# Kernel optimization log

Hardware: AMD Instinct MI355X
Metric: run time of the kernel (lower is better)

Reference implementation:

```python
import jax, jax.numpy as jnp
import numpy as np

B, T, D, H, F = 8, 1024, 512, 8, 2048
DK = D // H
EPS = 1e-3  # Keras LayerNormalization default epsilon
NEG = -1e9


def layer_norm(x, g, b):
    mu = jnp.mean(x, axis=-1, keepdims=True)
    var = jnp.mean(jnp.square(x - mu), axis=-1, keepdims=True)
    return (x - mu) * jax.lax.rsqrt(var + EPS) * g + b


def setup_inputs() -> dict:
    key = jax.random.key(0)
    ks = jax.random.split(key, 16)
    s = 1.0 / np.sqrt(D)
    sf = 1.0 / np.sqrt(F)
    x = jax.random.normal(ks[0], (B, T, D), dtype=jnp.float32)
    # binary attention mask (1 = attend). Random block-sparse-ish pattern.
    mask = (jax.random.uniform(ks[1], (B, 1, T, T)) > 0.15).astype(jnp.float32)
    return {
        "x": x,
        "mask": mask,
        "ln_in_g": jnp.ones((D,), jnp.float32),
        "ln_in_b": jnp.zeros((D,), jnp.float32),
        "Wq": jax.random.normal(ks[2], (D, D), jnp.float32) * s,
        "bq": jnp.zeros((D,), jnp.float32),
        "Wk": jax.random.normal(ks[3], (D, D), jnp.float32) * s,
        "bk": jnp.zeros((D,), jnp.float32),
        "Wv": jax.random.normal(ks[4], (D, D), jnp.float32) * s,
        "bv": jnp.zeros((D,), jnp.float32),
        "ln1_g": jnp.ones((D,), jnp.float32),
        "ln1_b": jnp.zeros((D,), jnp.float32),
        "W1": jax.random.normal(ks[5], (D, F), jnp.float32) * s,
        "b1": jnp.zeros((F,), jnp.float32),
        "W2": jax.random.normal(ks[6], (F, D), jnp.float32) * sf,
        "b2": jnp.zeros((D,), jnp.float32),
        "ln2_g": jnp.ones((D,), jnp.float32),
        "ln2_b": jnp.zeros((D,), jnp.float32),
    }


def reference(x, mask, ln_in_g, ln_in_b, Wq, bq, Wk, bk, Wv, bv,
              ln1_g, ln1_b, W1, b1, W2, b2, ln2_g, ln2_b):
    bs = x.shape[0]
    h = layer_norm(x, ln_in_g, ln_in_b)                      # [B,T,D]
    # QKV projections, split heads -> [B,H,T,DK]
    q = (h @ Wq + bq).reshape(bs, -1, H, DK).transpose(0, 2, 1, 3)
    k = (h @ Wk + bk).reshape(bs, -1, H, DK).transpose(0, 2, 1, 3)
    v = (h @ Wv + bv).reshape(bs, -1, H, DK).transpose(0, 2, 1, 3)
    scores = jnp.einsum('bhtd,bhsd->bhts', q, k) / np.sqrt(DK)
    scores = scores + NEG * (1.0 - mask)                     # additive mask
    probs = jax.nn.softmax(scores, axis=-1)                  # dropout: identity at inference
    attn = jnp.einsum('bhts,bhsd->bhtd', probs, v)
    attn = attn.transpose(0, 2, 1, 3).reshape(bs, -1, H * DK)
    # residual with ORIGINAL inputs (pre-ln_in), as in call() -> attend(inputs,...)
    attn = attn + x
    a = layer_norm(attn, ln1_g, ln1_b)
    f = jax.nn.relu(a @ W1 + b1) @ W2 + b2
    out = layer_norm(f + a, ln2_g, ln2_b)
    return out
```

## Files before the change

### kernel.cpp

```cpp
#include <hip/hip_runtime.h>

typedef unsigned short u16;
typedef unsigned long long u64;
typedef __bf16 bf16x8 __attribute__((ext_vector_type(8)));
typedef float f32x4 __attribute__((ext_vector_type(4)));

#define B_ 8
#define T_ 1024
#define D_ 512
#define H_ 8
#define DK_ 64
#define F_ 2048

__device__ __forceinline__ u16 f2bf(float f) {
    unsigned u = __float_as_uint(f);
    u += 0x7fffu + ((u >> 16) & 1u);
    return (u16)(u >> 16);
}

__global__ __launch_bounds__(256) void prep_wqkv(
    const float* __restrict__ Wq, const float* __restrict__ Wk, const float* __restrict__ Wv,
    const float* __restrict__ bq, const float* __restrict__ bk, const float* __restrict__ bv,
    u16* __restrict__ WT, float* __restrict__ bias)
{
    __shared__ u16 t[64][72];
    const int k0 = blockIdx.x * 64;
    const int n0 = blockIdx.y * 64;
    const float* W = (n0 < 512) ? Wq : (n0 < 1024 ? Wk : Wv);
    const int nb = n0 & 511;
    const int tid = threadIdx.x;
    const int r = tid >> 2, c4 = (tid & 3) * 16;
    const float* src = W + (size_t)(k0 + r) * 512 + nb + c4;
#pragma unroll
    for (int j = 0; j < 16; j += 4) {
        float4 v = *(const float4*)(src + j);
        t[r][c4 + j]     = f2bf(v.x);
        t[r][c4 + j + 1] = f2bf(v.y);
        t[r][c4 + j + 2] = f2bf(v.z);
        t[r][c4 + j + 3] = f2bf(v.w);
    }
    if (k0 == 0 && tid < 64) {
        int n = n0 + tid;
        bias[n] = (n < 512) ? bq[n] : (n < 1024 ? bk[n - 512] : bv[n - 1024]);
    }
    __syncthreads();
    u16 tmp[16];
#pragma unroll
    for (int j = 0; j < 16; ++j) tmp[j] = t[c4 + j][r];
    u16* dst = WT + (size_t)(n0 + r) * 512 + k0 + c4;
    *(uint4*)dst       = *(uint4*)&tmp[0];
    *(uint4*)(dst + 8) = *(uint4*)&tmp[8];
}

__global__ __launch_bounds__(256) void transcvt(
    const float* __restrict__ W, u16* __restrict__ WT, int K, int N)
{
    __shared__ u16 t[64][72];
    const int k0 = blockIdx.x * 64;
    const int n0 = blockIdx.y * 64;
    const int tid = threadIdx.x;
    const int r = tid >> 2, c4 = (tid & 3) * 16;
    const float* src = W + (size_t)(k0 + r) * N + n0 + c4;
#pragma unroll
    for (int j = 0; j < 16; j += 4) {
        float4 v = *(const float4*)(src + j);
        t[r][c4 + j]     = f2bf(v.x);
        t[r][c4 + j + 1] = f2bf(v.y);
        t[r][c4 + j + 2] = f2bf(v.z);
        t[r][c4 + j + 3] = f2bf(v.w);
    }
    __syncthreads();
    u16 tmp[16];
#pragma unroll
    for (int j = 0; j < 16; ++j) tmp[j] = t[c4 + j][r];
    u16* dst = WT + (size_t)(n0 + r) * K + k0 + c4;
    *(uint4*)dst       = *(uint4*)&tmp[0];
    *(uint4*)(dst + 8) = *(uint4*)&tmp[8];
}

__global__ __launch_bounds__(256) void maskbits(
    const float* __restrict__ mask, u64* __restrict__ Mb)
{
    int gw = (blockIdx.x * 256 + threadIdx.x) >> 6;
    int lane = threadIdx.x & 63;
#pragma unroll
    for (int i = 0; i < 16; ++i) {
        size_t chunk = (size_t)gw * 16 + i;
        float v = mask[chunk * 64 + lane];
        u64 bm = __ballot(v > 0.5f);
        if (lane == 0) Mb[chunk] = bm;
    }
}

__global__ __launch_bounds__(256) void ln_kernel(
    const float* __restrict__ X, const float* __restrict__ R,
    const float* __restrict__ g, const float* __restrict__ bt,
    u16* __restrict__ ob, float* __restrict__ of)
{
    int wave = threadIdx.x >> 6, lane = threadIdx.x & 63;
    int row = blockIdx.x * 4 + wave;
    size_t base = (size_t)row * D_ + lane * 8;
    float v[8];
    float4 a0 = *(const float4*)(X + base);
    float4 a1 = *(const float4*)(X + base + 4);
    v[0]=a0.x; v[1]=a0.y; v[2]=a0.z; v[3]=a0.w;
    v[4]=a1.x; v[5]=a1.y; v[6]=a1.z; v[7]=a1.w;
    if (R) {
        float4 r0 = *(const float4*)(R + base);
        float4 r1 = *(const float4*)(R + base + 4);
        v[0]+=r0.x; v[1]+=r0.y; v[2]+=r0.z; v[3]+=r0.w;
        v[4]+=r1.x; v[5]+=r1.y; v[6]+=r1.z; v[7]+=r1.w;
    }
    float s = 0.f, q = 0.f;
#pragma unroll
    for (int j = 0; j < 8; ++j) { s += v[j]; q += v[j] * v[j]; }
#pragma unroll
    for (int off = 32; off > 0; off >>= 1) {
        s += __shfl_xor(s, off);
        q += __shfl_xor(q, off);
    }
    float mu = s * (1.0f / D_);
    float var = q * (1.0f / D_) - mu * mu;
    float rstd = rsqrtf(var + 1e-3f);
    int c0 = lane * 8;
    float y[8];
#pragma unroll
    for (int j = 0; j < 8; ++j) y[j] = (v[j] - mu) * rstd * g[c0 + j] + bt[c0 + j];
    if (ob) {
        u16 t[8];
#pragma unroll
        for (int j = 0; j < 8; ++j) t[j] = f2bf(y[j]);
        *(uint4*)(ob + base) = *(uint4*)t;
    }
    if (of) {
        float4 o0, o1;
        o0.x=y[0]; o0.y=y[1]; o0.z=y[2]; o0.w=y[3];
        o1.x=y[4]; o1.y=y[5]; o1.z=y[6]; o1.w=y[7];
        *(float4*)(of + base) = o0;
        *(float4*)(of + base + 4) = o1;
    }
}

template<int BN, int RELU, int OUTBF, int WRITE_VT>
__global__ __launch_bounds__(256) void gemm_mt(
    const u16* __restrict__ A, const u16* __restrict__ BT,
    const float* __restrict__ bias, u16* __restrict__ Cb,
    float* __restrict__ Cf, u16* __restrict__ Vt, int M, int N, int K)
{
    constexpr int NI = BN / 32;
    __shared__ u16 As[128 * 32];
    __shared__ u16 Bs[BN * 32];
    const int tid = threadIdx.x;
    const int wave = tid >> 6, lane = tid & 63;
    const int quad = lane >> 4, l16 = lane & 15;
    const int wr = wave >> 1, wc = wave & 1;
    const int rowBase = blockIdx.y * 128;
    const int colBase = blockIdx.x * BN;
    const int lr = lane >> 2;
    const int lc = (lane & 3) * 8;
    f32x4 acc[4][NI] = {};
    for (int k0 = 0; k0 < K; k0 += 32) {
        __syncthreads();
#pragma unroll
        for (int c = 0; c < 2; ++c) {
            int chunk = wave * 2 + c;
            const u16* gp = A + (size_t)(rowBase + chunk * 16 + lr) * K + k0 + lc;
            __builtin_amdgcn_global_load_lds(
                (const __attribute__((address_space(1))) unsigned int*)gp,
                (__attribute__((address_space(3))) unsigned int*)&As[chunk * 512],
                16, 0, 0);
        }
#pragma unroll
        for (int c = 0; c < BN / 64; ++c) {
            int chunk = wave * (BN / 64) + c;
            const u16* gp = BT + (size_t)(colBase + chunk * 16 + lr) * K + k0 + lc;
            __builtin_amdgcn_global_load_lds(
                (const __attribute__((address_space(1))) unsigned int*)gp,
                (__attribute__((address_space(3))) unsigned int*)&Bs[chunk * 512],
                16, 0, 0);
        }
        __syncthreads();
        bf16x8 af[4], bfr[NI];
#pragma unroll
        for (int i = 0; i < 4; ++i)
            af[i] = *(const bf16x8*)&As[(wr * 64 + i * 16 + l16) * 32 + quad * 8];
#pragma unroll
        for (int j = 0; j < NI; ++j)
            bfr[j] = *(const bf16x8*)&Bs[(wc * (BN / 2) + j * 16 + l16) * 32 + quad * 8];
#pragma unroll
        for (int i = 0; i < 4; ++i)
#pragma unroll
            for (int j = 0; j < NI; ++j)
                acc[i][j] = __builtin_amdgcn_mfma_f32_16x16x32_bf16(af[i], bfr[j], acc[i][j], 0, 0, 0);
    }
#pragma unroll
    for (int i = 0; i < 4; ++i) {
        int row0 = rowBase + wr * 64 + i * 16 + quad * 4;
#pragma unroll
        for (int j = 0; j < NI; ++j) {
            int col = colBase + wc * (BN / 2) + j * 16 + l16;
            float bv = bias[col];
#pragma unroll
            for (int r = 0; r < 4; ++r) {
                float v = acc[i][j][r] + bv;
                if (RELU) v = fmaxf(v, 0.0f);
                if (OUTBF) Cb[(size_t)(row0 + r) * N + col] = f2bf(v);
                else       Cf[(size_t)(row0 + r) * N + col] = v;
                if (WRITE_VT && col >= 1024) {
                    int hv = col - 1024;
                    int row = row0 + r;
                    Vt[((size_t)((row >> 10) * 8 + (hv >> 6)) * 64 + (hv & 63)) * T_ + (row & 1023)] = f2bf(v);
                }
            }
        }
    }
}

__global__ __launch_bounds__(256) void attn_kernel(
    const u16* __restrict__ QKV, const u16* __restrict__ Vt,
    const u64* __restrict__ Mb, float* __restrict__ Out)
{
    const int flat = blockIdx.x + 16 * (blockIdx.y + 8 * blockIdx.z);
    const int xcd = flat & 7, slot = flat >> 3;
    const int bh = xcd * 8 + (slot >> 4);
    const int qt = slot & 15;
    const int b = bh >> 3, h = bh & 7;
    const int qBase = qt * 64;
    const int tid = threadIdx.x;
    const int wave = tid >> 6, lane = tid & 63;
    const int quad = lane >> 4, l16 = lane & 15;
    __shared__ u16 Ks[64][72];
    __shared__ u16 Vs[64][72];
    __shared__ u16 Ps[4][16][72];

    const int qRow = qBase + wave * 16 + l16;
    const u16* qptr = QKV + ((size_t)(b * T_) + qRow) * (3 * D_) + h * DK_;
    bf16x8 qf0 = *(const bf16x8*)(qptr + quad * 8);
    bf16x8 qf1 = *(const bf16x8*)(qptr + 32 + quad * 8);

    float l_i[4] = {0.f, 0.f, 0.f, 0.f};
    f32x4 o[4] = {{0,0,0,0},{0,0,0,0},{0,0,0,0},{0,0,0,0}};

    const int sr = tid >> 2;
    const int sc = (tid & 3) * 8;
    const u16* Kg = QKV + (size_t)(b * T_) * (3 * D_) + D_ + h * DK_;
    const u16* Vg = Vt + (size_t)(b * H_ + h) * DK_ * T_;
    const u64* Mg = Mb + ((size_t)(b * T_) + qBase + wave * 16 + quad * 4) * (T_ / 64);

    uint4 kb0 = *(const uint4*)(Kg + (size_t)sr * (3 * D_) + sc);
    uint4 kb1 = *(const uint4*)(Kg + (size_t)sr * (3 * D_) + sc + 32);
    uint4 vb0 = *(const uint4*)(Vg + (size_t)sr * T_ + sc);
    uint4 vb1 = *(const uint4*)(Vg + (size_t)sr * T_ + sc + 32);

    for (int s0 = 0; s0 < T_; s0 += 64) {
        __syncthreads();
        *(uint4*)&Ks[sr][sc]      = kb0;
        *(uint4*)&Ks[sr][sc + 32] = kb1;
        *(uint4*)&Vs[sr][sc]      = vb0;
        *(uint4*)&Vs[sr][sc + 32] = vb1;
        __syncthreads();
        if (s0 + 64 < T_) {
            int s1 = s0 + 64;
            kb0 = *(const uint4*)(Kg + (size_t)(s1 + sr) * (3 * D_) + sc);
            kb1 = *(const uint4*)(Kg + (size_t)(s1 + sr) * (3 * D_) + sc + 32);
            vb0 = *(const uint4*)(Vg + (size_t)sr * T_ + s1 + sc);
            vb1 = *(const uint4*)(Vg + (size_t)sr * T_ + s1 + sc + 32);
        }

        u64 m64[4];
#pragma unroll
        for (int r = 0; r < 4; ++r) m64[r] = Mg[(size_t)r * (T_ / 64) + (s0 >> 6)];

#pragma unroll
        for (int n = 0; n < 4; ++n) {
            f32x4 s4 = {0.f, 0.f, 0.f, 0.f};
            bf16x8 kf0 = *(const bf16x8*)&Ks[n * 16 + l16][quad * 8];
            bf16x8 kf1 = *(const bf16x8*)&Ks[n * 16 + l16][32 + quad * 8];
            s4 = __builtin_amdgcn_mfma_f32_16x16x32_bf16(qf0, kf0, s4, 0, 0, 0);
            s4 = __builtin_amdgcn_mfma_f32_16x16x32_bf16(qf1, kf1, s4, 0, 0, 0);
#pragma unroll
            for (int r = 0; r < 4; ++r) {
                float p = __expf(fmaf(s4[r], 0.125f, -10.0f));
                p = ((m64[r] >> (n * 16 + l16)) & 1ull) ? p : 0.0f;
                l_i[r] += p;
                Ps[wave][quad * 4 + r][n * 16 + l16] = f2bf(p);
            }
        }
        bf16x8 pf0 = *(const bf16x8*)&Ps[wave][l16][quad * 8];
        bf16x8 pf1 = *(const bf16x8*)&Ps[wave][l16][32 + quad * 8];
#pragma unroll
        for (int dt = 0; dt < 4; ++dt) {
            bf16x8 vf0 = *(const bf16x8*)&Vs[dt * 16 + l16][quad * 8];
            bf16x8 vf1 = *(const bf16x8*)&Vs[dt * 16 + l16][32 + quad * 8];
            o[dt] = __builtin_amdgcn_mfma_f32_16x16x32_bf16(pf0, vf0, o[dt], 0, 0, 0);
            o[dt] = __builtin_amdgcn_mfma_f32_16x16x32_bf16(pf1, vf1, o[dt], 0, 0, 0);
        }
    }
#pragma unroll
    for (int off = 1; off < 16; off <<= 1) {
#pragma unroll
        for (int r = 0; r < 4; ++r) l_i[r] += __shfl_xor(l_i[r], off);
    }
    float inv[4];
#pragma unroll
    for (int r = 0; r < 4; ++r) inv[r] = 1.0f / l_i[r];
    const int orow = qBase + wave * 16 + quad * 4;
    float* Ob = Out + ((size_t)(b * T_) + orow) * D_ + h * DK_;
#pragma unroll
    for (int dt = 0; dt < 4; ++dt) {
#pragma unroll
        for (int r = 0; r < 4; ++r)
            Ob[(size_t)r * D_ + dt * 16 + l16] = o[dt][r] * inv[r];
    }
}

extern "C" void kernel_launch(void* const* d_in, const int* in_sizes, int n_in,
                              void* d_out, int out_size, void* d_ws, size_t ws_size,
                              hipStream_t stream)
{
    const float* x       = (const float*)d_in[0];
    const float* mask    = (const float*)d_in[1];
    const float* ln_in_g = (const float*)d_in[2];
    const float* ln_in_b = (const float*)d_in[3];
    const float* Wq      = (const float*)d_in[4];
    const float* bq      = (const float*)d_in[5];
    const float* Wk      = (const float*)d_in[6];
    const float* bk      = (const float*)d_in[7];
    const float* Wv      = (const float*)d_in[8];
    const float* bv      = (const float*)d_in[9];
    const float* ln1_g   = (const float*)d_in[10];
    const float* ln1_b   = (const float*)d_in[11];
    const float* W1      = (const float*)d_in[12];
    const float* b1      = (const float*)d_in[13];
    const float* W2      = (const float*)d_in[14];
    const float* b2      = (const float*)d_in[15];
    const float* ln2_g   = (const float*)d_in[16];
    const float* ln2_b   = (const float*)d_in[17];
    float* out = (float*)d_out;

    char* ws = (char*)d_ws;
    size_t off = 0;
    auto alloc = [&](size_t bytes) -> void* {
        void* p = ws + off;
        off = (off + bytes + 255) & ~(size_t)255;
        return p;
    };
    u16*   WqkvT   = (u16*)alloc((size_t)1536 * 512 * 2);
    u16*   W1T     = (u16*)alloc((size_t)2048 * 512 * 2);
    u16*   W2T     = (u16*)alloc((size_t)512 * 2048 * 2);
    float* bias_q  = (float*)alloc(1536 * 4);
    u64*   Mb      = (u64*)alloc((size_t)B_ * T_ * (T_ / 64) * 8);
    u16*   h_bf    = (u16*)alloc((size_t)8192 * 512 * 2);
    u16*   QKV     = (u16*)alloc((size_t)8192 * 1536 * 2);
    u16*   Vt      = (u16*)alloc((size_t)B_ * H_ * DK_ * T_ * 2);
    float* attn    = (float*)alloc((size_t)8192 * 512 * 4);
    u16*   a_bf    = (u16*)alloc((size_t)8192 * 512 * 2);
    float* a_f     = (float*)alloc((size_t)8192 * 512 * 4);
    u16*   f1      = (u16*)alloc((size_t)8192 * 2048 * 2);
    float* f2      = (float*)alloc((size_t)8192 * 512 * 4);
    if (off > ws_size) return;

    prep_wqkv<<<dim3(8, 24), 256, 0, stream>>>(Wq, Wk, Wv, bq, bk, bv, WqkvT, bias_q);
    transcvt<<<dim3(512 / 64, 2048 / 64), 256, 0, stream>>>(W1, W1T, 512, 2048);
    transcvt<<<dim3(2048 / 64, 512 / 64), 256, 0, stream>>>(W2, W2T, 2048, 512);
    maskbits<<<2048, 256, 0, stream>>>(mask, Mb);

    ln_kernel<<<2048, 256, 0, stream>>>(x, nullptr, ln_in_g, ln_in_b, h_bf, nullptr);

    gemm_mt<128, 0, 1, 1><<<dim3(1536 / 128, 8192 / 128), 256, 0, stream>>>(
        h_bf, WqkvT, bias_q, QKV, nullptr, Vt, 8192, 1536, 512);

    attn_kernel<<<dim3(T_ / 64, H_, B_), 256, 0, stream>>>(QKV, Vt, Mb, attn);

    ln_kernel<<<2048, 256, 0, stream>>>(attn, x, ln1_g, ln1_b, a_bf, a_f);

    gemm_mt<128, 1, 1, 0><<<dim3(2048 / 128, 8192 / 128), 256, 0, stream>>>(
        a_bf, W1T, b1, f1, nullptr, nullptr, 8192, 2048, 512);

    gemm_mt<64, 0, 0, 0><<<dim3(512 / 64, 8192 / 128), 256, 0, stream>>>(
        f1, W2T, b2, nullptr, f2, nullptr, 8192, 512, 2048);

    ln_kernel<<<2048, 256, 0, stream>>>(f2, a_f, ln2_g, ln2_b, nullptr, out);
}
```

Measured before the change: 316.8 us.

## Double-buffer GEMM LDS tiles, merge prep kernels, skip redundant V writes

The GEMM kernel now keeps two LDS buffers and issues the global-to-LDS loads for the next K step before computing on the current one, so memory latency can overlap the MFMA work and one barrier per iteration is dropped. The four weight/mask preprocessing kernels are merged into one launch to cut launch overhead. The QKV GEMM no longer writes the V columns into the packed QKV buffer, since attention reads V from the transposed copy. Double buffering doubles LDS use per block and may lower occupancy. There is also a possible race: the prefetch into the other buffer has no wait before the next barrier, so correctness depends on the compiler inserting vmcnt waits.

Measured after the change: 301.5 us. 1.05x faster.

```diff
diff --git a/kernel.cpp b/kernel.cpp
--- a/kernel.cpp
+++ b/kernel.cpp
@@ -18,19 +18,13 @@
     return (u16)(u >> 16);
 }
 
-__global__ __launch_bounds__(256) void prep_wqkv(
-    const float* __restrict__ Wq, const float* __restrict__ Wk, const float* __restrict__ Wv,
-    const float* __restrict__ bq, const float* __restrict__ bk, const float* __restrict__ bv,
-    u16* __restrict__ WT, float* __restrict__ bias)
-{
-    __shared__ u16 t[64][72];
-    const int k0 = blockIdx.x * 64;
-    const int n0 = blockIdx.y * 64;
-    const float* W = (n0 < 512) ? Wq : (n0 < 1024 ? Wk : Wv);
-    const int nb = n0 & 511;
+__device__ __forceinline__ void tile_transcvt(
+    const float* __restrict__ W, u16* __restrict__ WT, int K, int N, int k0, int n0,
+    u16 (*t)[72])
+{
     const int tid = threadIdx.x;
     const int r = tid >> 2, c4 = (tid & 3) * 16;
-    const float* src = W + (size_t)(k0 + r) * 512 + nb + c4;
+    const float* src = W + (size_t)(k0 + r) * N + n0 + c4;
 #pragma unroll
     for (int j = 0; j < 16; j += 4) {
         float4 v = *(const float4*)(src + j);
@@ -39,36 +33,6 @@
         t[r][c4 + j + 2] = f2bf(v.z);
         t[r][c4 + j + 3] = f2bf(v.w);
     }
-    if (k0 == 0 && tid < 64) {
-        int n = n0 + tid;
-        bias[n] = (n < 512) ? bq[n] : (n < 1024 ? bk[n - 512] : bv[n - 1024]);
-    }
-    __syncthreads();
-    u16 tmp[16];
-#pragma unroll
-    for (int j = 0; j < 16; ++j) tmp[j] = t[c4 + j][r];
-    u16* dst = WT + (size_t)(n0 + r) * 512 + k0 + c4;
-    *(uint4*)dst       = *(uint4*)&tmp[0];
-    *(uint4*)(dst + 8) = *(uint4*)&tmp[8];
-}
-
-__global__ __launch_bounds__(256) void transcvt(
-    const float* __restrict__ W, u16* __restrict__ WT, int K, int N)
-{
-    __shared__ u16 t[64][72];
-    const int k0 = blockIdx.x * 64;
-    const int n0 = blockIdx.y * 64;
-    const int tid = threadIdx.x;
-    const int r = tid >> 2, c4 = (tid & 3) * 16;
-    const float* src = W + (size_t)(k0 + r) * N + n0 + c4;
-#pragma unroll
-    for (int j = 0; j < 16; j += 4) {
-        float4 v = *(const float4*)(src + j);
-        t[r][c4 + j]     = f2bf(v.x);
-        t[r][c4 + j + 1] = f2bf(v.y);
-        t[r][c4 + j + 2] = f2bf(v.z);
-        t[r][c4 + j + 3] = f2bf(v.w);
-    }
     __syncthreads();
     u16 tmp[16];
 #pragma unroll
@@ -78,17 +42,59 @@
     *(uint4*)(dst + 8) = *(uint4*)&tmp[8];
 }
 
-__global__ __launch_bounds__(256) void maskbits(
-    const float* __restrict__ mask, u64* __restrict__ Mb)
-{
-    int gw = (blockIdx.x * 256 + threadIdx.x) >> 6;
-    int lane = threadIdx.x & 63;
-#pragma unroll
-    for (int i = 0; i < 16; ++i) {
-        size_t chunk = (size_t)gw * 16 + i;
-        float v = mask[chunk * 64 + lane];
-        u64 bm = __ballot(v > 0.5f);
-        if (lane == 0) Mb[chunk] = bm;
+__global__ __launch_bounds__(256) void prep_all(
+    const float* __restrict__ Wq, const float* __restrict__ Wk, const float* __restrict__ Wv,
+    const float* __restrict__ bq, const float* __restrict__ bk, const float* __restrict__ bv,
+    const float* __restrict__ W1, const float* __restrict__ W2,
+    const float* __restrict__ mask,
+    u16* __restrict__ WqkvT, u16* __restrict__ W1T, u16* __restrict__ W2T,
+    float* __restrict__ bias, u64* __restrict__ Mb)
+{
+    __shared__ u16 t[64][72];
+    const int blk = blockIdx.x;
+    const int tid = threadIdx.x;
+    if (blk < 192) {
+        const int k0 = (blk & 7) * 64;
+        const int n0 = (blk >> 3) * 64;
+        const float* W = (n0 < 512) ? Wq : (n0 < 1024 ? Wk : Wv);
+        if (k0 == 0 && tid < 64) {
+            int n = n0 + tid;
+            bias[n] = (n < 512) ? bq[n] : (n < 1024 ? bk[n - 512] : bv[n - 1024]);
+        }
+        const int r = tid >> 2, c4 = (tid & 3) * 16;
+        const float* src = W + (size_t)(k0 + r) * 512 + (n0 & 511) + c4;
+#pragma unroll
+        for (int j = 0; j < 16; j += 4) {
+            float4 v = *(const float4*)(src + j);
+            t[r][c4 + j]     = f2bf(v.x);
+            t[r][c4 + j + 1] = f2bf(v.y);
+            t[r][c4 + j + 2] = f2bf(v.z);
+            t[r][c4 + j + 3] = f2bf(v.w);
+        }
+        __syncthreads();
+        u16 tmp[16];
+#pragma unroll
+        for (int j = 0; j < 16; ++j) tmp[j] = t[c4 + j][r];
+        u16* dst = WqkvT + (size_t)(n0 + r) * 512 + k0 + c4;
+        *(uint4*)dst       = *(uint4*)&tmp[0];
+        *(uint4*)(dst + 8) = *(uint4*)&tmp[8];
+    } else if (blk < 448) {
+        const int idx = blk - 192;
+        tile_transcvt(W1, W1T, 512, 2048, (idx & 7) * 64, (idx >> 3) * 64, t);
+    } else if (blk < 704) {
+        const int idx = blk - 448;
+        tile_transcvt(W2, W2T, 2048, 512, (idx & 31) * 64, (idx >> 5) * 64, t);
+    } else {
+        const int idx = blk - 704;
+        int gw = (idx * 256 + tid) >> 6;
+        int lane = tid & 63;
+#pragma unroll
+        for (int i = 0; i < 16; ++i) {
+            size_t chunk = (size_t)gw * 16 + i;
+            float v = mask[chunk * 64 + lane];
+            u64 bm = __ballot(v > 0.5f);
+            if (lane == 0) Mb[chunk] = bm;
+        }
     }
 }
 
@@ -142,14 +148,14 @@
 }
 
 template<int BN, int RELU, int OUTBF, int WRITE_VT>
-__global__ __launch_bounds__(256) void gemm_mt(
+__global__ __launch_bounds__(256) void gemm_db(
     const u16* __restrict__ A, const u16* __restrict__ BT,
     const float* __restrict__ bias, u16* __restrict__ Cb,
     float* __restrict__ Cf, u16* __restrict__ Vt, int M, int N, int K)
 {
     constexpr int NI = BN / 32;
-    __shared__ u16 As[128 * 32];
-    __shared__ u16 Bs[BN * 32];
+    __shared__ u16 As[2][128 * 32];
+    __shared__ u16 Bs[2][BN * 32];
     const int tid = threadIdx.x;
     const int wave = tid >> 6, lane = tid & 63;
     const int quad = lane >> 4, l16 = lane & 15;
@@ -158,35 +164,43 @@
     const int colBase = blockIdx.x * BN;
     const int lr = lane >> 2;
     const int lc = (lane & 3) * 8;
-    f32x4 acc[4][NI] = {};
-    for (int k0 = 0; k0 < K; k0 += 32) {
-        __syncthreads();
+    const u16* Abase = A  + (size_t)(rowBase + lr) * K + lc;
+    const u16* Bbase = BT + (size_t)(colBase + lr) * K + lc;
+
+    auto stage = [&](int k0, int buf) {
 #pragma unroll
         for (int c = 0; c < 2; ++c) {
             int chunk = wave * 2 + c;
-            const u16* gp = A + (size_t)(rowBase + chunk * 16 + lr) * K + k0 + lc;
+            const u16* gp = Abase + (size_t)(chunk * 16) * K + k0;
             __builtin_amdgcn_global_load_lds(
                 (const __attribute__((address_space(1))) unsigned int*)gp,
-                (__attribute__((address_space(3))) unsigned int*)&As[chunk * 512],
+                (__attribute__((address_space(3))) unsigned int*)&As[buf][chunk * 512],
                 16, 0, 0);
         }
 #pragma unroll
         for (int c = 0; c < BN / 64; ++c) {
             int chunk = wave * (BN / 64) + c;
-            const u16* gp = BT + (size_t)(colBase + chunk * 16 + lr) * K + k0 + lc;
+            const u16* gp = Bbase + (size_t)(chunk * 16) * K + k0;
             __builtin_amdgcn_global_load_lds(
                 (const __attribute__((address_space(1))) unsigned int*)gp,
-                (__attribute__((address_space(3))) unsigned int*)&Bs[chunk * 512],
+                (__attribute__((address_space(3))) unsigned int*)&Bs[buf][chunk * 512],
                 16, 0, 0);
         }
+    };
+
+    f32x4 acc[4][NI] = {};
+    stage(0, 0);
+    for (int k0 = 0; k0 < K; k0 += 32) {
+        const int buf = (k0 >> 5) & 1;
         __syncthreads();
+        if (k0 + 32 < K) stage(k0 + 32, buf ^ 1);
         bf16x8 af[4], bfr[NI];
 #pragma unroll
         for (int i = 0; i < 4; ++i)
-            af[i] = *(const bf16x8*)&As[(wr * 64 + i * 16 + l16) * 32 + quad * 8];
+            af[i] = *(const bf16x8*)&As[buf][(wr * 64 + i * 16 + l16) * 32 + quad * 8];
 #pragma unroll
         for (int j = 0; j < NI; ++j)
-            bfr[j] = *(const bf16x8*)&Bs[(wc * (BN / 2) + j * 16 + l16) * 32 + quad * 8];
+            bfr[j] = *(const bf16x8*)&Bs[buf][(wc * (BN / 2) + j * 16 + l16) * 32 + quad * 8];
 #pragma unroll
         for (int i = 0; i < 4; ++i)
 #pragma unroll
@@ -204,12 +218,14 @@
             for (int r = 0; r < 4; ++r) {
                 float v = acc[i][j][r] + bv;
                 if (RELU) v = fmaxf(v, 0.0f);
-                if (OUTBF) Cb[(size_t)(row0 + r) * N + col] = f2bf(v);
-                else       Cf[(size_t)(row0 + r) * N + col] = v;
                 if (WRITE_VT && col >= 1024) {
                     int hv = col - 1024;
                     int row = row0 + r;
                     Vt[((size_t)((row >> 10) * 8 + (hv >> 6)) * 64 + (hv & 63)) * T_ + (row & 1023)] = f2bf(v);
+                } else if (OUTBF) {
+                    Cb[(size_t)(row0 + r) * N + col] = f2bf(v);
+                } else {
+                    Cf[(size_t)(row0 + r) * N + col] = v;
                 }
             }
         }
@@ -360,24 +376,22 @@
     float* f2      = (float*)alloc((size_t)8192 * 512 * 4);
     if (off > ws_size) return;
 
-    prep_wqkv<<<dim3(8, 24), 256, 0, stream>>>(Wq, Wk, Wv, bq, bk, bv, WqkvT, bias_q);
-    transcvt<<<dim3(512 / 64, 2048 / 64), 256, 0, stream>>>(W1, W1T, 512, 2048);
-    transcvt<<<dim3(2048 / 64, 512 / 64), 256, 0, stream>>>(W2, W2T, 2048, 512);
-    maskbits<<<2048, 256, 0, stream>>>(mask, Mb);
+    prep_all<<<2752, 256, 0, stream>>>(Wq, Wk, Wv, bq, bk, bv, W1, W2, mask,
+                                       WqkvT, W1T, W2T, bias_q, Mb);
 
     ln_kernel<<<2048, 256, 0, stream>>>(x, nullptr, ln_in_g, ln_in_b, h_bf, nullptr);
 
-    gemm_mt<128, 0, 1, 1><<<dim3(1536 / 128, 8192 / 128), 256, 0, stream>>>(
+    gemm_db<128, 0, 1, 1><<<dim3(1536 / 128, 8192 / 128), 256, 0, stream>>>(
         h_bf, WqkvT, bias_q, QKV, nullptr, Vt, 8192, 1536, 512);
 
     attn_kernel<<<dim3(T_ / 64, H_, B_), 256, 0, stream>>>(QKV, Vt, Mb, attn);
 
     ln_kernel<<<2048, 256, 0, stream>>>(attn, x, ln1_g, ln1_b, a_bf, a_f);
 
-    gemm_mt<128, 1, 1, 0><<<dim3(2048 / 128, 8192 / 128), 256, 0, stream>>>(
+    gemm_db<128, 1, 1, 0><<<dim3(2048 / 128, 8192 / 128), 256, 0, stream>>>(
         a_bf, W1T, b1, f1, nullptr, nullptr, 8192, 2048, 512);
 
-    gemm_mt<64, 0, 0, 0><<<dim3(512 / 64, 8192 / 128), 256, 0, stream>>>(
+    gemm_db<64, 0, 0, 0><<<dim3(512 / 64, 8192 / 128), 256, 0, stream>>>(
         f1, W2T, b2, nullptr, f2, nullptr, 8192, 512, 2048);
 
     ln_kernel<<<2048, 256, 0, stream>>>(f2, a_f, ln2_g, ln2_b, nullptr, out);
```
